# Performance work log

Measured on AMD Instinct MI355X. Metric: run time of the kernel, lower is better.

Reference implementation:

```python
import jax, jax.numpy as jnp
import numpy as np

L = 10


def setup_inputs() -> dict:
    key = jax.random.key(0)
    ks = jax.random.split(key, L + 1)
    N = 1_000_000
    inp = {"points": jax.random.normal(ks[0], (N, 3), dtype=jnp.float32)}
    inp["cob_1"] = jax.random.normal(ks[1], (3, 3), dtype=jnp.float32)
    for l in range(2, L + 1):
        # [2l+1, 3*(2l-1)] change-of-basis matrix for angular order l
        inp[f"cob_{l}"] = jax.random.normal(ks[l], (2 * l + 1, 3 * (2 * l - 1)), dtype=jnp.float32)
    return inp


def _harmonic_forward(points, cobs):
    # points: [..., 3]; cobs: list of L matrices (cob_1 .. cob_L)
    shape = points.shape[:-1]
    f0 = jnp.ones(shape + (1,), dtype=points.dtype)
    # order-1 feature: [..., 3]
    f1 = jnp.einsum('...i,ji->...j', points, cobs[0])
    feats = [f0, f1]
    prev = f1
    for l in range(2, L + 1):
        cob = cobs[l - 1]  # [2l+1, 3*(2l-1)]
        # outer product of previous order feature with order-1 feature, flattened
        f = jnp.einsum('...i,...j->...ij', prev, f1).reshape(shape + (-1,))  # [..., 3*(2l-1)]
        f = jnp.einsum('...i,ji->...j', f, cob)  # [..., 2l+1]
        feats.append(f)
        prev = f
    return jnp.concatenate(feats, axis=-1)  # [..., (L+1)^2]


def reference(points, cob_1, cob_2, cob_3, cob_4, cob_5, cob_6, cob_7, cob_8, cob_9, cob_10):
    cobs = [cob_1, cob_2, cob_3, cob_4, cob_5, cob_6, cob_7, cob_8, cob_9, cob_10]
    return _harmonic_forward(points, cobs)
```

## Files before the change

### kernel.cpp

```cpp
#include <hip/hip_runtime.h>

#define BS 256
#define NFEAT 121


__device__ __forceinline__ float dot3(const float* __restrict__ c, float x, float y, float z) {
    return fmaf(c[2], z, fmaf(c[1], y, c[0] * x));
}

template<int LL, bool UPDATE_PREV>
__device__ __forceinline__ void step_l(const float* __restrict__ cob,
                                       float* __restrict__ srow, int colofs,
                                       float f1x, float f1y, float f1z,
                                       float* __restrict__ prev) {
    constexpr int IN  = 2 * LL - 1;
    constexpr int OUT = 2 * LL + 1;
    #pragma unroll 1
    for (int j = 0; j < OUT; ++j) {
        const float* __restrict__ crow = cob + j * (3 * IN);
        float acc = 0.f;
        #pragma unroll
        for (int a = 0; a < IN; ++a) {
            float s = dot3(crow + 3 * a, f1x, f1y, f1z);
            acc = fmaf(prev[a], s, acc);
        }
        srow[colofs + j] = acc;
    }
    if (UPDATE_PREV) {
        #pragma unroll
        for (int j = 0; j < OUT; ++j) prev[j] = srow[colofs + j];
    }
}

template<int W, int STRIDE, int CBASE>
__device__ __forceinline__ void flush_phase(const float* __restrict__ sbuf,
                                            float* __restrict__ out,
                                            long long p0, int nvalid, int t) {
    const int total = nvalid * W;
    for (int idx = t; idx < total; idx += BS) {
        const int r = idx / W;
        const int c = idx - r * W;
        out[(p0 + r) * (long long)NFEAT + CBASE + c] = sbuf[r * STRIDE + c];
    }
}

__global__ __launch_bounds__(BS) void harmonic_kernel(
    const float* __restrict__ points,
    const float* __restrict__ cob1,  const float* __restrict__ cob2,
    const float* __restrict__ cob3,  const float* __restrict__ cob4,
    const float* __restrict__ cob5,  const float* __restrict__ cob6,
    const float* __restrict__ cob7,  const float* __restrict__ cob8,
    const float* __restrict__ cob9,  const float* __restrict__ cob10,
    float* __restrict__ out, int N) {
    __shared__ float sbuf[BS * 45];

    const int t = threadIdx.x;
    const long long p0 = (long long)blockIdx.x * BS;
    const long long p  = p0 + t;
    const bool active = p < (long long)N;
    long long nv = (long long)N - p0;
    const int nvalid = nv > BS ? BS : (int)nv;

    float px = 0.f, py = 0.f, pz = 0.f;
    if (active) {
        px = points[p * 3 + 0];
        py = points[p * 3 + 1];
        pz = points[p * 3 + 2];
    }

    const float f1x = dot3(cob1 + 0, px, py, pz);
    const float f1y = dot3(cob1 + 3, px, py, pz);
    const float f1z = dot3(cob1 + 6, px, py, pz);

    float prev[21];
    prev[0] = f1x; prev[1] = f1y; prev[2] = f1z;

    {
        float* srow = sbuf + t * 37;
        srow[0] = 1.f;
        srow[1] = f1x; srow[2] = f1y; srow[3] = f1z;
        step_l<2, true>(cob2, srow, 4,  f1x, f1y, f1z, prev);
        step_l<3, true>(cob3, srow, 9,  f1x, f1y, f1z, prev);
        step_l<4, true>(cob4, srow, 16, f1x, f1y, f1z, prev);
        step_l<5, true>(cob5, srow, 25, f1x, f1y, f1z, prev);
    }
    __syncthreads();
    flush_phase<36, 37, 0>(sbuf, out, p0, nvalid, t);
    __syncthreads();

    {
        float* srow = sbuf + t * 45;
        step_l<6, true>(cob6, srow, 0,  f1x, f1y, f1z, prev);
        step_l<7, true>(cob7, srow, 13, f1x, f1y, f1z, prev);
        step_l<8, true>(cob8, srow, 28, f1x, f1y, f1z, prev);
    }
    __syncthreads();
    flush_phase<45, 45, 36>(sbuf, out, p0, nvalid, t);
    __syncthreads();

    {
        float* srow = sbuf + t * 41;
        step_l<9,  true >(cob9,  srow, 0,  f1x, f1y, f1z, prev);
        step_l<10, false>(cob10, srow, 19, f1x, f1y, f1z, prev);
    }
    __syncthreads();
    flush_phase<40, 41, 81>(sbuf, out, p0, nvalid, t);
}

extern "C" void kernel_launch(void* const* d_in, const int* in_sizes, int n_in,
                              void* d_out, int out_size, void* d_ws, size_t ws_size,
                              hipStream_t stream) {
    const float* points = (const float*)d_in[0];
    const float* cob[10];
    for (int i = 0; i < 10; ++i) cob[i] = (const float*)d_in[1 + i];
    float* out = (float*)d_out;
    const int N = in_sizes[0] / 3;

    const int grid = (N + BS - 1) / BS;
    harmonic_kernel<<<grid, BS, 0, stream>>>(
        points,
        cob[0], cob[1], cob[2], cob[3], cob[4],
        cob[5], cob[6], cob[7], cob[8], cob[9],
        out, N);
}
```

Before: 785.9 us.

## Flush harmonic outputs per wavefront to drop block barriers and shrink LDS

```diff
diff --git a/kernel.cpp b/kernel.cpp
--- a/kernel.cpp
+++ b/kernel.cpp
@@ -2,6 +2,7 @@
 
 #define BS 256
 #define NFEAT 121
+#define SST 21
 
 
 __device__ __forceinline__ float dot3(const float* __restrict__ c, float x, float y, float z) {
@@ -10,9 +11,9 @@
 
 template<int LL, bool UPDATE_PREV>
 __device__ __forceinline__ void step_l(const float* __restrict__ cob,
-                                       float* __restrict__ srow, int colofs,
+                                       float* srow, int colofs,
                                        float f1x, float f1y, float f1z,
-                                       float* __restrict__ prev) {
+                                       float* prev) {
     constexpr int IN  = 2 * LL - 1;
     constexpr int OUT = 2 * LL + 1;
     #pragma unroll 1
@@ -32,15 +33,32 @@
     }
 }
 
-template<int W, int STRIDE, int CBASE>
-__device__ __forceinline__ void flush_phase(const float* __restrict__ sbuf,
-                                            float* __restrict__ out,
-                                            long long p0, int nvalid, int t) {
-    const int total = nvalid * W;
-    for (int idx = t; idx < total; idx += BS) {
-        const int r = idx / W;
-        const int c = idx - r * W;
-        out[(p0 + r) * (long long)NFEAT + CBASE + c] = sbuf[r * STRIDE + c];
+template<int W>
+__device__ __forceinline__ void wave_flush(const float* slab,
+                                           float* __restrict__ outw,
+                                           int wrows, int lane) {
+    constexpr int RPI   = 64 / W;
+    constexpr int LANES = RPI * W;
+    constexpr int ITERS = (64 + RPI - 1) / RPI;
+    const int lr = lane / W;
+    const int lc = lane - lr * W;
+    if (lane < LANES) {
+        const float* sp = slab + lr * SST + lc;
+        float* __restrict__ gp = outw + lr * NFEAT + lc;
+        if (wrows == 64) {
+            #pragma unroll
+            for (int k = 0; k < ITERS; ++k) {
+                const bool safe = (k * RPI + RPI - 1) < 64;
+                if (safe || (k * RPI + lr) < 64)
+                    gp[k * RPI * NFEAT] = sp[k * RPI * SST];
+            }
+        } else {
+            #pragma unroll
+            for (int k = 0; k < ITERS; ++k) {
+                if (k * RPI + lr < wrows)
+                    gp[k * RPI * NFEAT] = sp[k * RPI * SST];
+            }
+        }
     }
 }
 
@@ -52,14 +70,18 @@
     const float* __restrict__ cob7,  const float* __restrict__ cob8,
     const float* __restrict__ cob9,  const float* __restrict__ cob10,
     float* __restrict__ out, int N) {
-    __shared__ float sbuf[BS * 45];
+    __shared__ float sbuf[BS * SST];
 
-    const int t = threadIdx.x;
-    const long long p0 = (long long)blockIdx.x * BS;
-    const long long p  = p0 + t;
+    const int t    = threadIdx.x;
+    const int lane = t & 63;
+    const int w    = t >> 6;
+    const long long p0    = (long long)blockIdx.x * BS;
+    const long long wbase = p0 + (w << 6);
+    const long long p     = wbase + lane;
     const bool active = p < (long long)N;
-    long long nv = (long long)N - p0;
-    const int nvalid = nv > BS ? BS : (int)nv;
+
+    long long nv = (long long)N - wbase;
+    const int wrows = nv >= 64 ? 64 : (nv > 0 ? (int)nv : 0);
 
     float px = 0.f, py = 0.f, pz = 0.f;
     if (active) {
@@ -75,36 +97,34 @@
     float prev[21];
     prev[0] = f1x; prev[1] = f1y; prev[2] = f1z;
 
-    {
-        float* srow = sbuf + t * 37;
-        srow[0] = 1.f;
-        srow[1] = f1x; srow[2] = f1y; srow[3] = f1z;
-        step_l<2, true>(cob2, srow, 4,  f1x, f1y, f1z, prev);
-        step_l<3, true>(cob3, srow, 9,  f1x, f1y, f1z, prev);
-        step_l<4, true>(cob4, srow, 16, f1x, f1y, f1z, prev);
-        step_l<5, true>(cob5, srow, 25, f1x, f1y, f1z, prev);
-    }
-    __syncthreads();
-    flush_phase<36, 37, 0>(sbuf, out, p0, nvalid, t);
-    __syncthreads();
+    float* srow       = sbuf + t * SST;
+    const float* slab = sbuf + (w << 6) * SST;
+    float* __restrict__ outw = out + wbase * NFEAT;
 
-    {
-        float* srow = sbuf + t * 45;
-        step_l<6, true>(cob6, srow, 0,  f1x, f1y, f1z, prev);
-        step_l<7, true>(cob7, srow, 13, f1x, f1y, f1z, prev);
-        step_l<8, true>(cob8, srow, 28, f1x, f1y, f1z, prev);
-    }
-    __syncthreads();
-    flush_phase<45, 45, 36>(sbuf, out, p0, nvalid, t);
-    __syncthreads();
+    srow[0] = 1.f;
+    srow[1] = f1x; srow[2] = f1y; srow[3] = f1z;
+    step_l<2, true>(cob2, srow, 4, f1x, f1y, f1z, prev);
+    step_l<3, true>(cob3, srow, 9, f1x, f1y, f1z, prev);
+    wave_flush<16>(slab, outw + 0, wrows, lane);
 
-    {
-        float* srow = sbuf + t * 41;
-        step_l<9,  true >(cob9,  srow, 0,  f1x, f1y, f1z, prev);
-        step_l<10, false>(cob10, srow, 19, f1x, f1y, f1z, prev);
-    }
-    __syncthreads();
-    flush_phase<40, 41, 81>(sbuf, out, p0, nvalid, t);
+    step_l<4, true>(cob4, srow, 0, f1x, f1y, f1z, prev);
+    step_l<5, true>(cob5, srow, 9, f1x, f1y, f1z, prev);
+    wave_flush<20>(slab, outw + 16, wrows, lane);
+
+    step_l<6, true>(cob6, srow, 0, f1x, f1y, f1z, prev);
+    wave_flush<13>(slab, outw + 36, wrows, lane);
+
+    step_l<7, true>(cob7, srow, 0, f1x, f1y, f1z, prev);
+    wave_flush<15>(slab, outw + 49, wrows, lane);
+
+    step_l<8, true>(cob8, srow, 0, f1x, f1y, f1z, prev);
+    wave_flush<17>(slab, outw + 64, wrows, lane);
+
+    step_l<9, true>(cob9, srow, 0, f1x, f1y, f1z, prev);
+    wave_flush<19>(slab, outw + 81, wrows, lane);
+
+    step_l<10, false>(cob10, srow, 0, f1x, f1y, f1z, prev);
+    wave_flush<21>(slab, outw + 100, wrows, lane);
 }
 
 extern "C" void kernel_launch(void* const* d_in, const int* in_sizes, int n_in,
```

After: 806.2 us. +2.6%, slower.

## Keep all features in registers and flush via single-wave chunked LDS staging

Applied to the files above, without the earlier changes.

```diff
diff --git a/kernel.cpp b/kernel.cpp
--- a/kernel.cpp
+++ b/kernel.cpp
@@ -1,46 +1,30 @@
 #include <hip/hip_runtime.h>
 
-#define BS 256
+#define BS 64
 #define NFEAT 121
+#define CHUNK 16
+#define NCHUNK 4
 
 
 __device__ __forceinline__ float dot3(const float* __restrict__ c, float x, float y, float z) {
     return fmaf(c[2], z, fmaf(c[1], y, c[0] * x));
 }
 
-template<int LL, bool UPDATE_PREV>
+template<int LL>
 __device__ __forceinline__ void step_l(const float* __restrict__ cob,
-                                       float* __restrict__ srow, int colofs,
-                                       float f1x, float f1y, float f1z,
-                                       float* __restrict__ prev) {
-    constexpr int IN  = 2 * LL - 1;
+                                       float* f, float f1x, float f1y, float f1z) {
+    constexpr int IN = 2 * LL - 1;
     constexpr int OUT = 2 * LL + 1;
-    #pragma unroll 1
+    constexpr int PB = (LL - 1) * (LL - 1);
+    constexpr int OB = LL * LL;
+    #pragma unroll
     for (int j = 0; j < OUT; ++j) {
         const float* __restrict__ crow = cob + j * (3 * IN);
         float acc = 0.f;
         #pragma unroll
-        for (int a = 0; a < IN; ++a) {
-            float s = dot3(crow + 3 * a, f1x, f1y, f1z);
-            acc = fmaf(prev[a], s, acc);
-        }
-        srow[colofs + j] = acc;
-    }
-    if (UPDATE_PREV) {
-        #pragma unroll
-        for (int j = 0; j < OUT; ++j) prev[j] = srow[colofs + j];
-    }
-}
-
-template<int W, int STRIDE, int CBASE>
-__device__ __forceinline__ void flush_phase(const float* __restrict__ sbuf,
-                                            float* __restrict__ out,
-                                            long long p0, int nvalid, int t) {
-    const int total = nvalid * W;
-    for (int idx = t; idx < total; idx += BS) {
-        const int r = idx / W;
-        const int c = idx - r * W;
-        out[(p0 + r) * (long long)NFEAT + CBASE + c] = sbuf[r * STRIDE + c];
+        for (int a = 0; a < IN; ++a)
+            acc = fmaf(f[PB + a], dot3(crow + 3 * a, f1x, f1y, f1z), acc);
+        f[OB + j] = acc;
     }
 }
 
@@ -52,14 +36,14 @@
     const float* __restrict__ cob7,  const float* __restrict__ cob8,
     const float* __restrict__ cob9,  const float* __restrict__ cob10,
     float* __restrict__ out, int N) {
-    __shared__ float sbuf[BS * 45];
+    __shared__ float sbuf[CHUNK * NFEAT];
 
-    const int t = threadIdx.x;
-    const long long p0 = (long long)blockIdx.x * BS;
-    const long long p  = p0 + t;
+    const int lane = threadIdx.x;
+    const long long wbase = (long long)blockIdx.x * BS;
+    const long long p = wbase + lane;
     const bool active = p < (long long)N;
-    long long nv = (long long)N - p0;
-    const int nvalid = nv > BS ? BS : (int)nv;
+    long long nv = (long long)N - wbase;
+    const int wrows = nv >= BS ? BS : (nv > 0 ? (int)nv : 0);
 
     float px = 0.f, py = 0.f, pz = 0.f;
     if (active) {
@@ -72,39 +56,57 @@
     const float f1y = dot3(cob1 + 3, px, py, pz);
     const float f1z = dot3(cob1 + 6, px, py, pz);
 
-    float prev[21];
-    prev[0] = f1x; prev[1] = f1y; prev[2] = f1z;
+    float f[NFEAT];
+    f[0] = 1.f; f[1] = f1x; f[2] = f1y; f[3] = f1z;
+    step_l<2>(cob2, f, f1x, f1y, f1z);
+    step_l<3>(cob3, f, f1x, f1y, f1z);
+    step_l<4>(cob4, f, f1x, f1y, f1z);
+    step_l<5>(cob5, f, f1x, f1y, f1z);
+    step_l<6>(cob6, f, f1x, f1y, f1z);
+    step_l<7>(cob7, f, f1x, f1y, f1z);
+    step_l<8>(cob8, f, f1x, f1y, f1z);
+    step_l<9>(cob9, f, f1x, f1y, f1z);
+    step_l<10>(cob10, f, f1x, f1y, f1z);
 
-    {
-        float* srow = sbuf + t * 37;
-        srow[0] = 1.f;
-        srow[1] = f1x; srow[2] = f1y; srow[3] = f1z;
-        step_l<2, true>(cob2, srow, 4,  f1x, f1y, f1z, prev);
-        step_l<3, true>(cob3, srow, 9,  f1x, f1y, f1z, prev);
-        step_l<4, true>(cob4, srow, 16, f1x, f1y, f1z, prev);
-        step_l<5, true>(cob5, srow, 25, f1x, f1y, f1z, prev);
+    float* __restrict__ outw = out + wbase * NFEAT;
+    const int myc = lane >> 4;
+    const int mr  = lane & 15;
+
+    if (wrows == BS) {
+        #pragma unroll 1
+        for (int c = 0; c < NCHUNK; ++c) {
+            if (myc == c) {
+                #pragma unroll
+                for (int col = 0; col < NFEAT; ++col)
+                    sbuf[mr * NFEAT + col] = f[col];
+            }
+            const int gbase = c * (CHUNK * NFEAT);
+            #pragma unroll
+            for (int k = 0; k < 30; ++k)
+                outw[gbase + k * 64 + lane] = sbuf[k * 64 + lane];
+            if (lane < 16)
+                outw[gbase + 1920 + lane] = sbuf[1920 + lane];
+        }
+    } else if (wrows > 0) {
+        #pragma unroll 1
+        for (int c = 0; c < NCHUNK; ++c) {
+            int vr = wrows - c * CHUNK;
+            if (vr <= 0) break;
+            if (vr > CHUNK) vr = CHUNK;
+            if (myc == c && mr < vr) {
+                #pragma unroll
+                for (int col = 0; col < NFEAT; ++col)
+                    sbuf[mr * NFEAT + col] = f[col];
+            }
+            const int gbase = c * (CHUNK * NFEAT);
+            const int nf = vr * NFEAT;
+            #pragma unroll 1
+            for (int k = 0; k < 31; ++k) {
+                const int idx = k * 64 + lane;
+                if (idx < nf) outw[gbase + idx] = sbuf[idx];
+            }
+        }
     }
-    __syncthreads();
-    flush_phase<36, 37, 0>(sbuf, out, p0, nvalid, t);
-    __syncthreads();
-
-    {
-        float* srow = sbuf + t * 45;
-        step_l<6, true>(cob6, srow, 0,  f1x, f1y, f1z, prev);
-        step_l<7, true>(cob7, srow, 13, f1x, f1y, f1z, prev);
-        step_l<8, true>(cob8, srow, 28, f1x, f1y, f1z, prev);
-    }
-    __syncthreads();
-    flush_phase<45, 45, 36>(sbuf, out, p0, nvalid, t);
-    __syncthreads();
-
-    {
-        float* srow = sbuf + t * 41;
-        step_l<9,  true >(cob9,  srow, 0,  f1x, f1y, f1z, prev);
-        step_l<10, false>(cob10, srow, 19, f1x, f1y, f1z, prev);
-    }
-    __syncthreads();
-    flush_phase<40, 41, 81>(sbuf, out, p0, nvalid, t);
 }
 
 extern "C" void kernel_launch(void* const* d_in, const int* in_sizes, int n_in,
```

Measured after the change: 726.1 us. -7.6%, faster.
